# Kernel tuning notes

Hardware: AMD Instinct MI355X
Metric: run time of the kernel (lower is better)

The kernel has to match this reference:

```python
import jax, jax.numpy as jnp
import numpy as np

NF, NV = 400000, 200000
C_IN, C_OUT, K, MULT = 64, 128, 27, 1
BN_EPS = 1e-5


def setup_inputs() -> dict:
    key = jax.random.key(0)
    ks = jax.random.split(key, 8)
    inputs = jax.random.normal(ks[0], (NF, C_IN), dtype=jnp.float32)
    filt_coeff = jax.random.uniform(ks[1], (NF, K), dtype=jnp.float32)
    face = jax.random.randint(ks[2], (NF, 3), 0, NV, dtype=jnp.int32)
    nf_count = jnp.ones((NV,), dtype=jnp.int32)
    vt_map = jnp.arange(NV, dtype=jnp.int64)
    # learned parameters (xavier-ish scale)
    spatial_weights = jax.random.normal(ks[3], (K, C_IN, MULT), dtype=jnp.float32) * np.sqrt(2.0 / (K * C_IN + MULT))
    depth_weights = jax.random.normal(ks[4], (C_IN * MULT, C_OUT), dtype=jnp.float32) * np.sqrt(2.0 / (C_IN * MULT + C_OUT))
    biases = jnp.zeros((1, C_OUT), dtype=jnp.float32)
    gamma = jnp.ones((C_OUT,), dtype=jnp.float32)
    beta = jnp.zeros((C_OUT,), dtype=jnp.float32)
    return {
        "inputs": inputs, "filt_coeff": filt_coeff, "face": face,
        "nf_count": nf_count, "vt_map": vt_map,
        "spatial_weights": spatial_weights, "depth_weights": depth_weights,
        "biases": biases, "gamma": gamma, "beta": beta,
    }


def reference(inputs, filt_coeff, face, nf_count, vt_map,
              spatial_weights, depth_weights, biases, gamma, beta):
    nv = nf_count.shape[0]
    nf = inputs.shape[0]
    # per-face mixture of spatial filters: [Nf, C_in, mult]
    w = jnp.einsum('fk,kcm->fcm', filt_coeff, spatial_weights)
    # per-face weighted features, flattened depthwise: [Nf, C_in*mult]
    contrib = (inputs[:, :, None] * w).reshape(nf, -1)
    # scatter each face's contribution to its 3 vertices
    idx = face.reshape(-1)                                  # [3*Nf]
    vals = jnp.broadcast_to(contrib[:, None, :], (nf, 3, contrib.shape[1])).reshape(3 * nf, -1)
    agg = jax.ops.segment_sum(vals, idx, num_segments=nv)    # [Nv, C_in*mult]
    # average by number of adjacent faces
    denom = jnp.maximum(nf_count, 1).astype(agg.dtype)[:, None]
    agg = agg / denom
    # reorder vertices per vt_map
    agg = agg[vt_map]
    # pointwise (depth) conv + bias + ReLU
    out = agg @ depth_weights + biases
    out = jax.nn.relu(out)
    # BatchNorm1d (training-mode batch statistics over vertices)
    mean = out.mean(axis=0)
    var = out.var(axis=0)
    out = (out - mean) * jax.lax.rsqrt(var + BN_EPS) * gamma + beta
    return out
```

## Files before the change

kernel.cpp:

```cpp
#include <hip/hip_runtime.h>
#include <hip/hip_bf16.h>

#define NFACE 400000
#define NVERT 200000
#define CIN 64
#define COUT 128
#define KF 27
#define BN_EPS 1e-5f

#define M_TOT (NFACE * 3)
#define NB    391
#define NBLK  256
#define CHUNK ((M_TOT + NBLK - 1) / NBLK)

typedef __attribute__((ext_vector_type(8))) short bf16x8;
typedef __attribute__((ext_vector_type(4))) float f32x4;
typedef __attribute__((ext_vector_type(8))) unsigned short ushort8;

__device__ __forceinline__ short f2bf(float x) {
    __hip_bfloat16 h = __float2bfloat16(x);
    return *reinterpret_cast<short*>(&h);
}
__device__ __forceinline__ float bf2f(unsigned short u) {
    union { unsigned int i; float f; } x; x.i = ((unsigned)u) << 16; return x.f;
}

__global__ __launch_bounds__(256) void prep_hist_k(
    const float* __restrict__ sw, const float* __restrict__ dw,
    short* __restrict__ swf, short* __restrict__ dwb,
    float* __restrict__ stats,
    const int* __restrict__ faceflat, int* __restrict__ blockcnt) {
    const int t = threadIdx.x;
    if (blockIdx.x == 0) {
#pragma unroll
        for (int j = 0; j < 8; ++j) stats[t + j * 256] = 0.f;
        {
            int cb = t >> 6, lane = t & 63;
            int ch = cb * 16 + (lane & 15);
#pragma unroll
            for (int j = 0; j < 8; ++j) {
                int k = (lane >> 4) * 8 + j;
                swf[t * 8 + j] = (k < KF) ? f2bf(sw[k * 64 + ch]) : (short)0;
            }
        }
#pragma unroll
        for (int p4 = 0; p4 < 4; ++p4) {
            int p = t + p4 * 256;
            int frag = p >> 6, lane = p & 63;
            int nb = frag >> 3, tt = (frag >> 1) & 3, kk = frag & 1;
            int col = nb * 64 + tt * 16 + (lane & 15);
#pragma unroll
            for (int j = 0; j < 8; ++j) {
                int k = kk * 32 + (lane >> 4) * 8 + j;
                dwb[(size_t)p * 8 + j] = f2bf(dw[k * 128 + col]);
            }
        }
    } else {
        __shared__ int h[512];
        const int blk = blockIdx.x - 1;
        for (int j = t; j < 512; j += 256) h[j] = 0;
        __syncthreads();
        int e0 = blk * CHUNK;
        int e1 = min(e0 + CHUNK, M_TOT);
        for (int e = e0 + t; e < e1; e += 256)
            atomicAdd(&h[faceflat[e] >> 9], 1);
        __syncthreads();
        for (int j = t; j < 512; j += 256) blockcnt[blk * 512 + j] = h[j];
    }
}

__global__ __launch_bounds__(256) void scan_k(int* __restrict__ blockcnt,
                                              int* __restrict__ bucket_start,
                                              int* __restrict__ row_off) {
    __shared__ int tot[512];
    __shared__ int bst[512];
    const int t = threadIdx.x;
    for (int b = t; b < 512; b += 256) {
        int acc = 0;
        if (b < NB)
            for (int k = 0; k < NBLK; ++k) acc += blockcnt[k * 512 + b];
        tot[b] = acc;
    }
    __syncthreads();
    if (t < 64) {
        int base8 = t * 8, loc[8], s = 0;
#pragma unroll
        for (int j = 0; j < 8; ++j) { loc[j] = s; s += tot[base8 + j]; }
        int v = s;
        for (int off = 1; off < 64; off <<= 1) {
            int u = __shfl_up(v, off);
            if (t >= off) v += u;
        }
        int excl = v - s;
#pragma unroll
        for (int j = 0; j < 8; ++j) bst[base8 + j] = excl + loc[j];
    }
    __syncthreads();
    for (int b = t; b < NB; b += 256) bucket_start[b] = bst[b];
    if (t == 0) { bucket_start[NB] = bst[NB]; row_off[NVERT] = M_TOT; }
    for (int b = t; b < NB; b += 256) {
        int acc = bst[b];
        for (int k = 0; k < NBLK; ++k) {
            int c = blockcnt[k * 512 + b];
            blockcnt[k * 512 + b] = acc;
            acc += c;
        }
    }
}

__global__ __launch_bounds__(256) void scat_k(const int* __restrict__ faceflat,
                                              const int* __restrict__ blockcnt,
                                              int2* __restrict__ pairs) {
    __shared__ int baseL[512];
    __shared__ int lc[512];
    const int t = threadIdx.x, blk = blockIdx.x;
    for (int j = t; j < 512; j += 256) { baseL[j] = blockcnt[blk * 512 + j]; lc[j] = 0; }
    __syncthreads();
    int e0 = blk * CHUNK;
    int e1 = min(e0 + CHUNK, M_TOT);
    for (int e = e0 + t; e < e1; e += 256) {
        int v = faceflat[e];
        int b = v >> 9;
        int l = atomicAdd(&lc[b], 1);
        pairs[baseL[b] + l] = make_int2(v, e / 3);
    }
}

__global__ __launch_bounds__(256) void csr_k(const int2* __restrict__ pairs,
                                             const int* __restrict__ bucket_start,
                                             int* __restrict__ row_off,
                                             int* __restrict__ csr) {
    __shared__ int cnt[512], esc[512], pc[512];
    const int t = threadIdx.x, b = blockIdx.x;
    const int p0 = bucket_start[b], p1 = bucket_start[b + 1];
    const int vbase = b << 9;
    for (int j = t; j < 512; j += 256) { cnt[j] = 0; pc[j] = 0; }
    __syncthreads();
    for (int i = p0 + t; i < p1; i += 256)
        atomicAdd(&cnt[pairs[i].x - vbase], 1);
    __syncthreads();
    if (t < 64) {
        int base8 = t * 8, loc[8], s = 0;
#pragma unroll
        for (int j = 0; j < 8; ++j) { loc[j] = s; s += cnt[base8 + j]; }
        int v = s;
        for (int off = 1; off < 64; off <<= 1) {
            int u = __shfl_up(v, off);
            if (t >= off) v += u;
        }
        int excl = v - s;
#pragma unroll
        for (int j = 0; j < 8; ++j) esc[base8 + j] = excl + loc[j];
    }
    __syncthreads();
    int nvb = min(512, NVERT - vbase);
    for (int j = t; j < nvb; j += 256) row_off[vbase + j] = p0 + esc[j];
    for (int i = p0 + t; i < p1; i += 256) {
        int lv = pairs[i].x - vbase;
        int l = atomicAdd(&pc[lv], 1);
        csr[p0 + esc[lv] + l] = pairs[i].y;
    }
}

__global__ __launch_bounds__(256, 4) void mix_k(
    const float* __restrict__ inputs,
    const float* __restrict__ filt,
    const short* __restrict__ swf,
    __hip_bfloat16* __restrict__ contrib)
{
    const int t    = threadIdx.x;
    const int lane = t & 63;
    const int wid  = t >> 6;
    const int fb   = blockIdx.x * 128;
    const int r    = lane & 15;
    const int qg   = lane >> 4;
    const int f0   = fb + wid * 32 + r;
    const int f1   = f0 + 16;

    bf16x8 afr[4];
#pragma unroll
    for (int cb = 0; cb < 4; ++cb)
        afr[cb] = *(const bf16x8*)&swf[(cb * 64 + lane) * 8];

    const int k0 = qg * 8;
    const size_t lim = (size_t)NFACE * KF - 8;
    size_t base0 = (size_t)f0 * KF + k0;
    size_t base1 = (size_t)f1 * KF + k0;
    bool cl0 = base0 > lim; if (cl0) base0 = lim;
    bool cl1 = base1 > lim; if (cl1) base1 = lim;
    f32x4 fa0 = __builtin_nontemporal_load((const f32x4*)&filt[base0]);
    f32x4 fq0 = __builtin_nontemporal_load((const f32x4*)&filt[base0 + 4]);
    f32x4 fa1 = __builtin_nontemporal_load((const f32x4*)&filt[base1]);
    f32x4 fq1 = __builtin_nontemporal_load((const f32x4*)&filt[base1 + 4]);

    f32x4 in0[4], in1[4];
#pragma unroll
    for (int cb = 0; cb < 4; ++cb) {
        int c0 = cb * 16 + qg * 4;
        in0[cb] = __builtin_nontemporal_load(
            (const f32x4*)&inputs[(size_t)f0 * 64 + c0]);
        in1[cb] = __builtin_nontemporal_load(
            (const f32x4*)&inputs[(size_t)f1 * 64 + c0]);
    }

    float wv0[8] = {fa0[0], fa0[1], fa0[2], fa0[3], fq0[0], fq0[1], fq0[2], fq0[3]};
    float wv1[8] = {fa1[0], fa1[1], fa1[2], fa1[3], fq1[0], fq1[1], fq1[2], fq1[3]};
    bf16x8 b0, b1;
#pragma unroll
    for (int j = 0; j < 8; ++j) {
        int k = k0 + j;
        float v0 = cl0 ? ((j < 3) ? wv0[j + 5] : 0.f) : ((k < KF) ? wv0[j] : 0.f);
        float v1 = cl1 ? ((j < 3) ? wv1[j + 5] : 0.f) : ((k < KF) ? wv1[j] : 0.f);
        b0[j] = f2bf(v0);
        b1[j] = f2bf(v1);
    }

    f32x4 acc0[4], acc1[4];
#pragma unroll
    for (int cb = 0; cb < 4; ++cb) {
        acc0[cb] = __builtin_amdgcn_mfma_f32_16x16x32_bf16(afr[cb], b0, (f32x4){0.f, 0.f, 0.f, 0.f}, 0, 0, 0);
        acc1[cb] = __builtin_amdgcn_mfma_f32_16x16x32_bf16(afr[cb], b1, (f32x4){0.f, 0.f, 0.f, 0.f}, 0, 0, 0);
    }

#pragma unroll
    for (int cb = 0; cb < 4; ++cb) {
        int c0 = cb * 16 + qg * 4;
        short4 o0, o1;
        o0.x = f2bf(in0[cb][0] * acc0[cb][0]);
        o0.y = f2bf(in0[cb][1] * acc0[cb][1]);
        o0.z = f2bf(in0[cb][2] * acc0[cb][2]);
        o0.w = f2bf(in0[cb][3] * acc0[cb][3]);
        o1.x = f2bf(in1[cb][0] * acc1[cb][0]);
        o1.y = f2bf(in1[cb][1] * acc1[cb][1]);
        o1.z = f2bf(in1[cb][2] * acc1[cb][2]);
        o1.w = f2bf(in1[cb][3] * acc1[cb][3]);
        *(short4*)((short*)contrib + (size_t)f0 * 64 + c0) = o0;
        *(short4*)((short*)contrib + (size_t)f1 * 64 + c0) = o1;
    }
}

#define BV 32
__global__ __launch_bounds__(256, 6) void pconv_k(
    const __hip_bfloat16* __restrict__ contrib,
    const int* __restrict__ row_off,
    const int* __restrict__ csr,
    const int* __restrict__ nf_count,
    const int* __restrict__ vt_map,
    const short* __restrict__ dwb,
    const float* __restrict__ bias,
    __hip_bfloat16* __restrict__ outb,
    float* __restrict__ stats)
{
    __shared__ float denL[BV];
    __shared__ int   offL[BV];
    __shared__ int   degL[BV];
    __shared__ int   flatL[BV][32];
    __shared__ __align__(16) short A[BV * 64];
    __shared__ __align__(16) short outL[BV * 128];

    const int t     = threadIdx.x;
    const int lane  = t & 63;
    const int wid   = t >> 6;
    const int vbase = blockIdx.x * BV;
    const unsigned short* ct = (const unsigned short*)contrib;

    if (t < BV) {
        int src = vt_map[vbase + t];
        denL[t] = 1.f / (float)max(nf_count[src], 1);
        int o = row_off[src];
        int d = row_off[src + 1] - o;
        offL[t] = o;
        degL[t] = d > 32 ? 32 : d;
    }
    __syncthreads();
#pragma unroll
    for (int r = 0; r < 4; ++r) {
        int i = t + r * 256;
        int row = i >> 5, j = i & 31;
        flatL[row][j] = (j < degL[row]) ? csr[offL[row] + j] : 0;
    }
    __syncthreads();

#pragma unroll
    for (int g = 0; g < 2; ++g) {
        const int q0 = wid * 8 + g * 4;
        const int n0 = degL[q0 + 0], n1 = degL[q0 + 1];
        const int n2 = degL[q0 + 2], n3 = degL[q0 + 3];
        int jm = max(max(n0, n1), max(n2, n3));
        float s0 = 0.f, s1 = 0.f, s2 = 0.f, s3 = 0.f;
        for (int j = 0; j < jm; j += 4) {
            int f00 = flatL[q0 + 0][j + 0], f01 = flatL[q0 + 0][j + 1];
            int f02 = flatL[q0 + 0][j + 2], f03 = flatL[q0 + 0][j + 3];
            int f10 = flatL[q0 + 1][j + 0], f11 = flatL[q0 + 1][j + 1];
            int f12 = flatL[q0 + 1][j + 2], f13 = flatL[q0 + 1][j + 3];
            int f20 = flatL[q0 + 2][j + 0], f21 = flatL[q0 + 2][j + 1];
            int f22 = flatL[q0 + 2][j + 2], f23 = flatL[q0 + 2][j + 3];
            int f30 = flatL[q0 + 3][j + 0], f31 = flatL[q0 + 3][j + 1];
            int f32_ = flatL[q0 + 3][j + 2], f33 = flatL[q0 + 3][j + 3];
            float v00 = bf2f(ct[(size_t)f00 * 64 + lane]);
            float v01 = bf2f(ct[(size_t)f01 * 64 + lane]);
            float v02 = bf2f(ct[(size_t)f02 * 64 + lane]);
            float v03 = bf2f(ct[(size_t)f03 * 64 + lane]);
            float v10 = bf2f(ct[(size_t)f10 * 64 + lane]);
            float v11 = bf2f(ct[(size_t)f11 * 64 + lane]);
            float v12 = bf2f(ct[(size_t)f12 * 64 + lane]);
            float v13 = bf2f(ct[(size_t)f13 * 64 + lane]);
            float v20 = bf2f(ct[(size_t)f20 * 64 + lane]);
            float v21 = bf2f(ct[(size_t)f21 * 64 + lane]);
            float v22 = bf2f(ct[(size_t)f22 * 64 + lane]);
            float v23 = bf2f(ct[(size_t)f23 * 64 + lane]);
            float v30 = bf2f(ct[(size_t)f30 * 64 + lane]);
            float v31 = bf2f(ct[(size_t)f31 * 64 + lane]);
            float v32 = bf2f(ct[(size_t)f32_ * 64 + lane]);
            float v33 = bf2f(ct[(size_t)f33 * 64 + lane]);
            s0 += ((j + 0 < n0) ? v00 : 0.f) + ((j + 1 < n0) ? v01 : 0.f)
                + ((j + 2 < n0) ? v02 : 0.f) + ((j + 3 < n0) ? v03 : 0.f);
            s1 += ((j + 0 < n1) ? v10 : 0.f) + ((j + 1 < n1) ? v11 : 0.f)
                + ((j + 2 < n1) ? v12 : 0.f) + ((j + 3 < n1) ? v13 : 0.f);
            s2 += ((j + 0 < n2) ? v20 : 0.f) + ((j + 1 < n2) ? v21 : 0.f)
                + ((j + 2 < n2) ? v22 : 0.f) + ((j + 3 < n2) ? v23 : 0.f);
            s3 += ((j + 0 < n3) ? v30 : 0.f) + ((j + 1 < n3) ? v31 : 0.f)
                + ((j + 2 < n3) ? v32 : 0.f) + ((j + 3 < n3) ? v33 : 0.f);
        }
        s0 *= denL[q0 + 0]; s1 *= denL[q0 + 1];
        s2 *= denL[q0 + 2]; s3 *= denL[q0 + 3];
#pragma unroll
        for (int r = 0; r < 4; ++r) {
            int q = q0 + r;
            float sv = (r == 0) ? s0 : (r == 1) ? s1 : (r == 2) ? s2 : s3;
            int swz = (lane & 7) | ((((lane >> 3) ^ (q & 7))) << 3);
            A[q * 64 + swz] = f2bf(sv);
        }
    }
    __syncthreads();

    const int mi = wid & 1;
    const int nbq = wid >> 1;
    f32x4 acc[4];
#pragma unroll
    for (int tt = 0; tt < 4; ++tt) acc[tt] = (f32x4){0.f, 0.f, 0.f, 0.f};
#pragma unroll
    for (int kk = 0; kk < 2; ++kk) {
        int row = mi * 16 + (lane & 15);
        int chunk = (kk * 4 + (lane >> 4)) ^ (row & 7);
        bf16x8 a = *(const bf16x8*)&A[row * 64 + chunk * 8];
#pragma unroll
        for (int tt = 0; tt < 4; ++tt) {
            int frag = (nbq * 4 + tt) * 2 + kk;
            bf16x8 b = *(const bf16x8*)&dwb[((size_t)frag * 64 + lane) * 8];
            acc[tt] = __builtin_amdgcn_mfma_f32_16x16x32_bf16(a, b, acc[tt], 0, 0, 0);
        }
    }

    float* st = stats + (blockIdx.x & 7) * 256;
#pragma unroll
    for (int tt = 0; tt < 4; ++tt) {
        int col = nbq * 64 + tt * 16 + (lane & 15);
        float bv = bias[col];
        float s = 0.f, s2 = 0.f;
#pragma unroll
        for (int i = 0; i < 4; ++i) {
            float o = fmaxf(acc[tt][i] + bv, 0.f);
            int row = mi * 16 + (lane >> 4) * 4 + i;
            outL[row * 128 + col] = f2bf(o);
            s  += o;
            s2 += o * o;
        }
        s  += __shfl_xor(s, 16);  s  += __shfl_xor(s, 32);
        s2 += __shfl_xor(s2, 16); s2 += __shfl_xor(s2, 32);
        if ((lane >> 4) == 0) {
            atomicAdd(&st[col], s);
            atomicAdd(&st[128 + col], s2);
        }
    }
    __syncthreads();

#pragma unroll
    for (int r = 0; r < 2; ++r) {
        int i = t + r * 256;
        ((int4*)&outb[(size_t)vbase * 128])[i] = ((const int4*)outL)[i];
    }
}

__global__ __launch_bounds__(256) void bn_k(
    const __hip_bfloat16* __restrict__ outb,
    float* __restrict__ out,
    const float* __restrict__ stats,
    const float* __restrict__ gamma,
    const float* __restrict__ beta)
{
    __shared__ float sc[128], sh[128];
    if (threadIdx.x < 128) {
        int c = threadIdx.x;
        float s = 0.f, s2 = 0.f;
#pragma unroll
        for (int r = 0; r < 8; ++r) {
            s  += stats[r * 256 + c];
            s2 += stats[r * 256 + 128 + c];
        }
        float mean = s / (float)NVERT;
        float var  = s2 / (float)NVERT - mean * mean;
        float inv  = rsqrtf(var + BN_EPS) * gamma[c];
        sc[c] = inv;
        sh[c] = beta[c] - mean * inv;
    }
    __syncthreads();

    const ushort8* ob8 = (const ushort8*)outb;
    size_t total8 = (size_t)NVERT * COUT / 8;
    for (size_t i = (size_t)blockIdx.x * 256 + threadIdx.x; i < total8;
         i += (size_t)gridDim.x * 256) {
        int c0 = (int)((i * 8) & 127);
        ushort8 u = ob8[i];
        f32x4 v0, v1;
        v0[0] = bf2f(u[0]) * sc[c0 + 0] + sh[c0 + 0];
        v0[1] = bf2f(u[1]) * sc[c0 + 1] + sh[c0 + 1];
        v0[2] = bf2f(u[2]) * sc[c0 + 2] + sh[c0 + 2];
        v0[3] = bf2f(u[3]) * sc[c0 + 3] + sh[c0 + 3];
        v1[0] = bf2f(u[4]) * sc[c0 + 4] + sh[c0 + 4];
        v1[1] = bf2f(u[5]) * sc[c0 + 5] + sh[c0 + 5];
        v1[2] = bf2f(u[6]) * sc[c0 + 6] + sh[c0 + 6];
        v1[3] = bf2f(u[7]) * sc[c0 + 7] + sh[c0 + 7];
        __builtin_nontemporal_store(v0, (f32x4*)&out[i * 8]);
        __builtin_nontemporal_store(v1, (f32x4*)&out[i * 8 + 4]);
    }
}

extern "C" void kernel_launch(void* const* d_in, const int* in_sizes, int n_in,
                              void* d_out, int out_size, void* d_ws, size_t ws_size,
                              hipStream_t stream) {
    const float* inputs   = (const float*)d_in[0];
    const float* filt     = (const float*)d_in[1];
    const int*   face     = (const int*)d_in[2];
    const int*   nf_count = (const int*)d_in[3];
    const int*   vt_map   = (const int*)d_in[4];
    const float* sw       = (const float*)d_in[5];
    const float* dw       = (const float*)d_in[6];
    const float* bias     = (const float*)d_in[7];
    const float* gamma    = (const float*)d_in[8];
    const float* beta     = (const float*)d_in[9];
    float* out = (float*)d_out;

    char* w = (char*)d_ws;
    float*          stats = (float*)w;
    short*          swf   = (short*)(w + 8192);
    short*          dwb   = (short*)(w + 16384);
    __hip_bfloat16* outb  = (__hip_bfloat16*)(w + 32768);

    char* o = (char*)d_out;
    __hip_bfloat16* contrib      = (__hip_bfloat16*)o;
    int2*           pairs        = (int2*)(o + 51200000);
    int*            csr          = (int*)(o + 60800000);
    int*            row_off      = (int*)(o + 65600000);
    int*            blockcnt     = (int*)(o + 66400256);
    int*            bucket_start = (int*)(o + 66924544);
    const int*      faceflat     = face;

    prep_hist_k<<<NBLK + 1, 256, 0, stream>>>(sw, dw, swf, dwb, stats,
                                              faceflat, blockcnt);
    scan_k<<<1, 256, 0, stream>>>(blockcnt, bucket_start, row_off);
    scat_k<<<NBLK, 256, 0, stream>>>(faceflat, blockcnt, pairs);
    csr_k<<<NB, 256, 0, stream>>>(pairs, bucket_start, row_off, csr);
    mix_k<<<NFACE / 128, 256, 0, stream>>>(inputs, filt, swf, contrib);
    pconv_k<<<NVERT / BV, 256, 0, stream>>>(contrib, row_off, csr, nf_count,
                                            vt_map, dwb, bias, outb, stats);
    bn_k<<<4096, 256, 0, stream>>>(outb, out, stats, gamma, beta);
}
```

Baseline: 189.8 us.

## Fuse histogram, weight prep and face mixing into one kernel launch

```diff
diff --git a/kernel.cpp b/kernel.cpp
--- a/kernel.cpp
+++ b/kernel.cpp
@@ -12,6 +12,7 @@
 #define NB    391
 #define NBLK  256
 #define CHUNK ((M_TOT + NBLK - 1) / NBLK)
+#define MIXBLK (NFACE / 128)
 
 typedef __attribute__((ext_vector_type(8))) short bf16x8;
 typedef __attribute__((ext_vector_type(4))) float f32x4;
@@ -25,24 +26,31 @@
     union { unsigned int i; float f; } x; x.i = ((unsigned)u) << 16; return x.f;
 }
 
-__global__ __launch_bounds__(256) void prep_hist_k(
+__global__ __launch_bounds__(256, 4) void k1_fused(
     const float* __restrict__ sw, const float* __restrict__ dw,
-    short* __restrict__ swf, short* __restrict__ dwb,
-    float* __restrict__ stats,
-    const int* __restrict__ faceflat, int* __restrict__ blockcnt) {
+    const float* __restrict__ inputs, const float* __restrict__ filt,
+    short* __restrict__ dwb, float* __restrict__ stats,
+    const int* __restrict__ faceflat, int* __restrict__ blockcnt,
+    __hip_bfloat16* __restrict__ contrib)
+{
     const int t = threadIdx.x;
-    if (blockIdx.x == 0) {
+    const int bid = blockIdx.x;
+
+    if (bid < NBLK) {
+        __shared__ int h[512];
+        for (int j = t; j < 512; j += 256) h[j] = 0;
+        __syncthreads();
+        int e0 = bid * CHUNK;
+        int e1 = min(e0 + CHUNK, M_TOT);
+        for (int e = e0 + t; e < e1; e += 256)
+            atomicAdd(&h[faceflat[e] >> 9], 1);
+        __syncthreads();
+        for (int j = t; j < 512; j += 256) blockcnt[bid * 512 + j] = h[j];
+        return;
+    }
+    if (bid == NBLK) {
 #pragma unroll
         for (int j = 0; j < 8; ++j) stats[t + j * 256] = 0.f;
-        {
-            int cb = t >> 6, lane = t & 63;
-            int ch = cb * 16 + (lane & 15);
-#pragma unroll
-            for (int j = 0; j < 8; ++j) {
-                int k = (lane >> 4) * 8 + j;
-                swf[t * 8 + j] = (k < KF) ? f2bf(sw[k * 64 + ch]) : (short)0;
-            }
-        }
 #pragma unroll
         for (int p4 = 0; p4 < 4; ++p4) {
             int p = t + p4 * 256;
@@ -55,123 +63,12 @@
                 dwb[(size_t)p * 8 + j] = f2bf(dw[k * 128 + col]);
             }
         }
-    } else {
-        __shared__ int h[512];
-        const int blk = blockIdx.x - 1;
-        for (int j = t; j < 512; j += 256) h[j] = 0;
-        __syncthreads();
-        int e0 = blk * CHUNK;
-        int e1 = min(e0 + CHUNK, M_TOT);
-        for (int e = e0 + t; e < e1; e += 256)
-            atomicAdd(&h[faceflat[e] >> 9], 1);
-        __syncthreads();
-        for (int j = t; j < 512; j += 256) blockcnt[blk * 512 + j] = h[j];
-    }
-}
-
-__global__ __launch_bounds__(256) void scan_k(int* __restrict__ blockcnt,
-                                              int* __restrict__ bucket_start,
-                                              int* __restrict__ row_off) {
-    __shared__ int tot[512];
-    __shared__ int bst[512];
-    const int t = threadIdx.x;
-    for (int b = t; b < 512; b += 256) {
-        int acc = 0;
-        if (b < NB)
-            for (int k = 0; k < NBLK; ++k) acc += blockcnt[k * 512 + b];
-        tot[b] = acc;
-    }
-    __syncthreads();
-    if (t < 64) {
-        int base8 = t * 8, loc[8], s = 0;
-#pragma unroll
-        for (int j = 0; j < 8; ++j) { loc[j] = s; s += tot[base8 + j]; }
-        int v = s;
-        for (int off = 1; off < 64; off <<= 1) {
-            int u = __shfl_up(v, off);
-            if (t >= off) v += u;
-        }
-        int excl = v - s;
-#pragma unroll
-        for (int j = 0; j < 8; ++j) bst[base8 + j] = excl + loc[j];
-    }
-    __syncthreads();
-    for (int b = t; b < NB; b += 256) bucket_start[b] = bst[b];
-    if (t == 0) { bucket_start[NB] = bst[NB]; row_off[NVERT] = M_TOT; }
-    for (int b = t; b < NB; b += 256) {
-        int acc = bst[b];
-        for (int k = 0; k < NBLK; ++k) {
-            int c = blockcnt[k * 512 + b];
-            blockcnt[k * 512 + b] = acc;
-            acc += c;
-        }
-    }
-}
-
-__global__ __launch_bounds__(256) void scat_k(const int* __restrict__ faceflat,
-                                              const int* __restrict__ blockcnt,
-                                              int2* __restrict__ pairs) {
-    __shared__ int baseL[512];
-    __shared__ int lc[512];
-    const int t = threadIdx.x, blk = blockIdx.x;
-    for (int j = t; j < 512; j += 256) { baseL[j] = blockcnt[blk * 512 + j]; lc[j] = 0; }
-    __syncthreads();
-    int e0 = blk * CHUNK;
-    int e1 = min(e0 + CHUNK, M_TOT);
-    for (int e = e0 + t; e < e1; e += 256) {
-        int v = faceflat[e];
-        int b = v >> 9;
-        int l = atomicAdd(&lc[b], 1);
-        pairs[baseL[b] + l] = make_int2(v, e / 3);
-    }
-}
-
-__global__ __launch_bounds__(256) void csr_k(const int2* __restrict__ pairs,
-                                             const int* __restrict__ bucket_start,
-                                             int* __restrict__ row_off,
-                                             int* __restrict__ csr) {
-    __shared__ int cnt[512], esc[512], pc[512];
-    const int t = threadIdx.x, b = blockIdx.x;
-    const int p0 = bucket_start[b], p1 = bucket_start[b + 1];
-    const int vbase = b << 9;
-    for (int j = t; j < 512; j += 256) { cnt[j] = 0; pc[j] = 0; }
-    __syncthreads();
-    for (int i = p0 + t; i < p1; i += 256)
-        atomicAdd(&cnt[pairs[i].x - vbase], 1);
-    __syncthreads();
-    if (t < 64) {
-        int base8 = t * 8, loc[8], s = 0;
-#pragma unroll
-        for (int j = 0; j < 8; ++j) { loc[j] = s; s += cnt[base8 + j]; }
-        int v = s;
-        for (int off = 1; off < 64; off <<= 1) {
-            int u = __shfl_up(v, off);
-            if (t >= off) v += u;
-        }
-        int excl = v - s;
-#pragma unroll
-        for (int j = 0; j < 8; ++j) esc[base8 + j] = excl + loc[j];
-    }
-    __syncthreads();
-    int nvb = min(512, NVERT - vbase);
-    for (int j = t; j < nvb; j += 256) row_off[vbase + j] = p0 + esc[j];
-    for (int i = p0 + t; i < p1; i += 256) {
-        int lv = pairs[i].x - vbase;
-        int l = atomicAdd(&pc[lv], 1);
-        csr[p0 + esc[lv] + l] = pairs[i].y;
-    }
-}
-
-__global__ __launch_bounds__(256, 4) void mix_k(
-    const float* __restrict__ inputs,
-    const float* __restrict__ filt,
-    const short* __restrict__ swf,
-    __hip_bfloat16* __restrict__ contrib)
-{
-    const int t    = threadIdx.x;
+        return;
+    }
+
     const int lane = t & 63;
     const int wid  = t >> 6;
-    const int fb   = blockIdx.x * 128;
+    const int fb   = (bid - NBLK - 1) * 128;
     const int r    = lane & 15;
     const int qg   = lane >> 4;
     const int f0   = fb + wid * 32 + r;
@@ -179,8 +76,14 @@
 
     bf16x8 afr[4];
 #pragma unroll
-    for (int cb = 0; cb < 4; ++cb)
-        afr[cb] = *(const bf16x8*)&swf[(cb * 64 + lane) * 8];
+    for (int cb = 0; cb < 4; ++cb) {
+        int ch = cb * 16 + r;
+#pragma unroll
+        for (int j = 0; j < 8; ++j) {
+            int k = qg * 8 + j;
+            afr[cb][j] = (k < KF) ? f2bf(sw[k * 64 + ch]) : (short)0;
+        }
+    }
 
     const int k0 = qg * 8;
     const size_t lim = (size_t)NFACE * KF - 8;
@@ -236,6 +139,99 @@
         o1.w = f2bf(in1[cb][3] * acc1[cb][3]);
         *(short4*)((short*)contrib + (size_t)f0 * 64 + c0) = o0;
         *(short4*)((short*)contrib + (size_t)f1 * 64 + c0) = o1;
+    }
+}
+
+__global__ __launch_bounds__(256) void scan_k(int* __restrict__ blockcnt,
+                                              int* __restrict__ bucket_start,
+                                              int* __restrict__ row_off) {
+    __shared__ int tot[512];
+    __shared__ int bst[512];
+    const int t = threadIdx.x;
+    for (int b = t; b < 512; b += 256) {
+        int acc = 0;
+        if (b < NB)
+            for (int k = 0; k < NBLK; ++k) acc += blockcnt[k * 512 + b];
+        tot[b] = acc;
+    }
+    __syncthreads();
+    if (t < 64) {
+        int base8 = t * 8, loc[8], s = 0;
+#pragma unroll
+        for (int j = 0; j < 8; ++j) { loc[j] = s; s += tot[base8 + j]; }
+        int v = s;
+        for (int off = 1; off < 64; off <<= 1) {
+            int u = __shfl_up(v, off);
+            if (t >= off) v += u;
+        }
+        int excl = v - s;
+#pragma unroll
+        for (int j = 0; j < 8; ++j) bst[base8 + j] = excl + loc[j];
+    }
+    __syncthreads();
+    for (int b = t; b < NB; b += 256) bucket_start[b] = bst[b];
+    if (t == 0) { bucket_start[NB] = bst[NB]; row_off[NVERT] = M_TOT; }
+    for (int b = t; b < NB; b += 256) {
+        int acc = bst[b];
+        for (int k = 0; k < NBLK; ++k) {
+            int c = blockcnt[k * 512 + b];
+            blockcnt[k * 512 + b] = acc;
+            acc += c;
+        }
+    }
+}
+
+__global__ __launch_bounds__(256) void scat_k(const int* __restrict__ faceflat,
+                                              const int* __restrict__ blockcnt,
+                                              int2* __restrict__ pairs) {
+    __shared__ int baseL[512];
+    __shared__ int lc[512];
+    const int t = threadIdx.x, blk = blockIdx.x;
+    for (int j = t; j < 512; j += 256) { baseL[j] = blockcnt[blk * 512 + j]; lc[j] = 0; }
+    __syncthreads();
+    int e0 = blk * CHUNK;
+    int e1 = min(e0 + CHUNK, M_TOT);
+    for (int e = e0 + t; e < e1; e += 256) {
+        int v = faceflat[e];
+        int b = v >> 9;
+        int l = atomicAdd(&lc[b], 1);
+        pairs[baseL[b] + l] = make_int2(v, e / 3);
+    }
+}
+
+__global__ __launch_bounds__(256) void csr_k(const int2* __restrict__ pairs,
+                                             const int* __restrict__ bucket_start,
+                                             int* __restrict__ row_off,
+                                             int* __restrict__ csr) {
+    __shared__ int cnt[512], esc[512], pc[512];
+    const int t = threadIdx.x, b = blockIdx.x;
+    const int p0 = bucket_start[b], p1 = bucket_start[b + 1];
+    const int vbase = b << 9;
+    for (int j = t; j < 512; j += 256) { cnt[j] = 0; pc[j] = 0; }
+    __syncthreads();
+    for (int i = p0 + t; i < p1; i += 256)
+        atomicAdd(&cnt[pairs[i].x - vbase], 1);
+    __syncthreads();
+    if (t < 64) {
+        int base8 = t * 8, loc[8], s = 0;
+#pragma unroll
+        for (int j = 0; j < 8; ++j) { loc[j] = s; s += cnt[base8 + j]; }
+        int v = s;
+        for (int off = 1; off < 64; off <<= 1) {
+            int u = __shfl_up(v, off);
+            if (t >= off) v += u;
+        }
+        int excl = v - s;
+#pragma unroll
+        for (int j = 0; j < 8; ++j) esc[base8 + j] = excl + loc[j];
+    }
+    __syncthreads();
+    int nvb = min(512, NVERT - vbase);
+    for (int j = t; j < nvb; j += 256) row_off[vbase + j] = p0 + esc[j];
+    for (int i = p0 + t; i < p1; i += 256) {
+        int lv = pairs[i].x - vbase;
+        int l = atomicAdd(&pc[lv], 1);
+        csr[p0 + esc[lv] + l] = pairs[i].y;
     }
 }
 
@@ -443,7 +439,6 @@
 
     char* w = (char*)d_ws;
     float*          stats = (float*)w;
-    short*          swf   = (short*)(w + 8192);
     short*          dwb   = (short*)(w + 16384);
     __hip_bfloat16* outb  = (__hip_bfloat16*)(w + 32768);
 
@@ -456,12 +451,11 @@
     int*            bucket_start = (int*)(o + 66924544);
     const int*      faceflat     = face;
 
-    prep_hist_k<<<NBLK + 1, 256, 0, stream>>>(sw, dw, swf, dwb, stats,
-                                              faceflat, blockcnt);
+    k1_fused<<<NBLK + 1 + MIXBLK, 256, 0, stream>>>(
+        sw, dw, inputs, filt, dwb, stats, faceflat, blockcnt, contrib);
     scan_k<<<1, 256, 0, stream>>>(blockcnt, bucket_start, row_off);
     scat_k<<<NBLK, 256, 0, stream>>>(faceflat, blockcnt, pairs);
     csr_k<<<NB, 256, 0, stream>>>(pairs, bucket_start, row_off, csr);
-    mix_k<<<NFACE / 128, 256, 0, stream>>>(inputs, filt, swf, contrib);
     pconv_k<<<NVERT / BV, 256, 0, stream>>>(contrib, row_off, csr, nf_count,
                                             vt_map, dwb, bias, outb, stats);
     bn_k<<<4096, 256, 0, stream>>>(outb, out, stats, gamma, beta);
```

Result: no change. 192.5 us (+1.4%).
